# Optimization experiments

Measured on AMD Instinct MI355X. Metric: run time of the kernel, lower is better.

The kernel has to match this reference:

```python
import jax, jax.numpy as jnp
import numpy as np


def _approx_match(xyz1, xyz2):
    """Faithful port of approxmatch_cpu/cuda (auction-style soft bipartite matching).

    xyz1: [b, n, 3], xyz2: [b, m, 3] -> (match [b, n, m], sq_dists [b, n, m])
    """
    b, n, _ = xyz1.shape
    m = xyz2.shape[1]
    factorl = max(n, m) // n  # integer division, as in the CUDA source
    factorr = max(n, m) // m

    # all-pairs squared distances  [b, n, m]
    d2 = jnp.sum((xyz1[:, :, None, :] - xyz2[:, None, :, :]) ** 2, axis=-1)

    # annealing schedule: j = 8 .. -1 -> level = -4^j ; j = -2 -> level = 0
    levels = jnp.asarray([-(4.0 ** j) for j in range(8, -2, -1)] + [0.0],
                         dtype=xyz1.dtype)

    satl0 = jnp.full((b, n), float(factorl), dtype=xyz1.dtype)  # row capacities
    satr0 = jnp.full((b, m), float(factorr), dtype=xyz1.dtype)  # col capacities
    match0 = jnp.zeros((b, n, m), dtype=xyz1.dtype)

    def step(carry, level):
        satl, satr, match = carry
        # weight = exp(level * d2) * saturatedr
        w = jnp.exp(level * d2) * satr[:, None, :]                       # [b,n,m]
        # row-normalize, scale by remaining row capacity
        w = w / (jnp.sum(w, axis=2, keepdims=True) + 1e-9) * satl[:, :, None]
        # column rescale by remaining column capacity
        ss = jnp.sum(w, axis=1) + 1e-9                                   # [b,m]
        w = w * (satr / ss)[:, None, :]
        # deplete capacities
        satl = jnp.maximum(satl - jnp.sum(w, axis=2), 0.0)
        satr = jnp.maximum(satr - jnp.sum(w, axis=1), 0.0)
        return (satl, satr, match + w), None

    (_, _, match), _ = jax.lax.scan(step, (satl0, satr0, match0), levels)
    return match, d2


def setup_inputs() -> dict:
    key = jax.random.key(0)
    k1, k2 = jax.random.split(key)
    b, n, m = 4, 4096, 4096
    return {
        "input1": jax.random.normal(k1, (b, n, 3), dtype=jnp.float32),
        "input2": jax.random.normal(k2, (b, m, 3), dtype=jnp.float32),
        "eps": 0,    # accepted but unused by the original Function
        "iters": 50, # accepted but unused by the original Function
    }


def reference(input1, input2, eps, iters):
    # eps / iters are ignored, matching EarthMoverDistanceFunction.apply(xyz1, xyz2)
    match, d2 = _approx_match(input1, input2)
    dist = jnp.sqrt(jnp.maximum(d2, 1e-12))  # matchcost uses euclidean (sqrt) distance
    return jnp.sum(match * dist, axis=(1, 2))  # cost per batch element, [b]
```

## Files before the change

### kernel.cpp

```cpp
#include <hip/hip_runtime.h>

#define BLOCK 256
#define IC    64
#define RPT   4
#define ROWS  (BLOCK*RPT)
#define RBLK  64

__device__ __forceinline__ float wave_reduce_add(float v) {
#pragma unroll
    for (int off = 32; off > 0; off >>= 1) v += __shfl_down(v, off, 64);
    return v;
}
__device__ __forceinline__ float lg2(float x) { return __builtin_amdgcn_logf(x); }
__device__ __forceinline__ float ex2(float x) { return __builtin_amdgcn_exp2f(x); }

__device__ __forceinline__ void load_rows(const float* p, float* x, float* y, float* z) {
    float4 v0 = *(const float4*)p;
    float4 v1 = *(const float4*)(p + 4);
    float4 v2 = *(const float4*)(p + 8);
    x[0]=v0.x; x[1]=v0.w; x[2]=v1.z; x[3]=v2.y;
    y[0]=v0.y; y[1]=v1.x; y[2]=v1.w; y[3]=v2.z;
    z[0]=v0.z; z[1]=v1.y; z[2]=v2.x; z[3]=v2.w;
}

__global__ __launch_bounds__(BLOCK)
void emd_init(float* __restrict__ satl, float* __restrict__ satr,
              float* __restrict__ out, float fl, float fr,
              int b, int n, int m) {
    int idx = blockIdx.x * blockDim.x + threadIdx.x;
    if (idx < b * n) satl[idx] = fl;
    if (idx < b * m) satr[idx] = fr;
    if (idx < b)     out[idx]  = 0.f;
}

__global__ __launch_bounds__(BLOCK, 4)
void emd_pass1(const float* __restrict__ xyz1, const float* __restrict__ xyz2,
               float* __restrict__ P1p, float ls, float wconst, float thr,
               int n, int m, int bn)
{
    __shared__ float4 sh[IC];
    const int bb = blockIdx.z, chunk = blockIdx.y;

    const int i0 = blockIdx.x * ROWS + threadIdx.x * RPT;
    float x[RPT], y[RPT], z[RPT], acc[RPT];
    load_rows(xyz1 + ((size_t)bb * n + i0) * 3, x, y, z);

    const float* x2 = xyz2 + (size_t)bb * m * 3;
    for (int t = threadIdx.x; t < IC; t += BLOCK) {
        int j = chunk * IC + t;
        sh[t] = make_float4(x2[3*j], x2[3*j+1], x2[3*j+2], wconst);
    }
    __syncthreads();

#pragma unroll
    for (int r = 0; r < RPT; ++r) acc[r] = 0.f;
#pragma unroll 2
    for (int tb = 0; tb < IC; tb += 4) {
        float4 q0 = sh[tb+0], q1 = sh[tb+1], q2 = sh[tb+2], q3 = sh[tb+3];
        float d0[RPT], d1[RPT], d2v[RPT], d3[RPT];
        float dmin = 1e30f;
#pragma unroll
        for (int r = 0; r < RPT; ++r) {
            float dx, dy, dz;
            dx=x[r]-q0.x; dy=y[r]-q0.y; dz=z[r]-q0.z; d0[r]=fmaf(dz,dz,fmaf(dy,dy,dx*dx));
            dx=x[r]-q1.x; dy=y[r]-q1.y; dz=z[r]-q1.z; d1[r]=fmaf(dz,dz,fmaf(dy,dy,dx*dx));
            dx=x[r]-q2.x; dy=y[r]-q2.y; dz=z[r]-q2.z; d2v[r]=fmaf(dz,dz,fmaf(dy,dy,dx*dx));
            dx=x[r]-q3.x; dy=y[r]-q3.y; dz=z[r]-q3.z; d3[r]=fmaf(dz,dz,fmaf(dy,dy,dx*dx));
            dmin = fminf(dmin, fminf(fminf(d0[r], d1[r]), fminf(d2v[r], d3[r])));
        }
        if (__any(dmin < thr)) {
#pragma unroll
            for (int r = 0; r < RPT; ++r) {
                acc[r] += ex2(fmaf(d0[r],  ls, q0.w));
                acc[r] += ex2(fmaf(d1[r],  ls, q1.w));
                acc[r] += ex2(fmaf(d2v[r], ls, q2.w));
                acc[r] += ex2(fmaf(d3[r],  ls, q3.w));
            }
        }
    }
    *(float4*)&P1p[(size_t)chunk * bn + (size_t)bb * n + i0] =
        make_float4(acc[0], acc[1], acc[2], acc[3]);
}

__global__ __launch_bounds__(BLOCK, 4)
void emd_pass2(const float* __restrict__ xyzO, const float* __restrict__ xyzS,
               const float* __restrict__ satlIn, float* __restrict__ satlOut,
               const float* __restrict__ aIn, float* __restrict__ aOut,
               const float* __restrict__ P1p, const float* __restrict__ P3a,
               const float* __restrict__ P3b, float* __restrict__ P2p,
               float* __restrict__ cost,
               float ls, float thr, int nO, int nS, int bnS, int bnO,
               int C4, int first)
{
    __shared__ float4 sh[IC];
    __shared__ float red[3][4][IC];
    const int bb = blockIdx.z, chunk = blockIdx.y;

    const int j0 = blockIdx.x * ROWS + threadIdx.x * RPT;
    float x[RPT], y[RPT], z[RPT], acc[RPT];
    load_rows(xyzO + ((size_t)bb * nO + j0) * 3, x, y, z);

    const int t6 = threadIdx.x & 63, g = threadIdx.x >> 6;
    const size_t ri = (size_t)bb * nS + chunk * IC + t6;
    {
        float ps = 0.f, pa = 0.f, pb = 0.f;
        const int c0 = g * C4;
        if (first) {
#pragma unroll 16
            for (int k = 0; k < C4; ++k) ps += P1p[(size_t)(c0 + k) * bnS + ri];
        } else {
#pragma unroll 16
            for (int k = 0; k < C4; ++k) {
                ps += P1p[(size_t)(c0 + k) * bnS + ri];
                pa += P3a[(size_t)(c0 + k) * bnS + ri];
                pb += P3b[(size_t)(c0 + k) * bnS + ri];
            }
        }
        red[0][g][t6] = ps; red[1][g][t6] = pa; red[2][g][t6] = pb;
    }
    __syncthreads();
    if (threadIdx.x < IC) {
        float rs = red[0][0][t6] + red[0][1][t6] + red[0][2][t6] + red[0][3][t6];
        float sl, costv = 0.f;
        if (first) {
            sl = satlIn[ri];
        } else {
            float s1 = red[1][0][t6] + red[1][1][t6] + red[1][2][t6] + red[1][3][t6];
            float s2 = red[2][0][t6] + red[2][1][t6] + red[2][2][t6] + red[2][3][t6];
            float ap = aIn[ri];
            sl = fmaxf(satlIn[ri] - ap * s1, 0.f);
            costv = ap * s2;
        }
        float av = sl / (rs + 1e-9f);
        if (blockIdx.x == 0) {
            satlOut[ri] = sl;
            aOut[ri]    = av;
            if (!first) {
                float cv = wave_reduce_add(costv);
                if (t6 == 0) atomicAdd(&cost[bb], cv);
            }
        }
        const float* xs = xyzS + ((size_t)bb * nS + chunk * IC + t6) * 3;
        sh[t6] = make_float4(xs[0], xs[1], xs[2], lg2(av));
    }
    __syncthreads();

#pragma unroll
    for (int r = 0; r < RPT; ++r) acc[r] = 0.f;
    if (thr < 1e29f) {
#pragma unroll 2
        for (int tb = 0; tb < IC; tb += 4) {
            float4 q0 = sh[tb+0], q1 = sh[tb+1], q2 = sh[tb+2], q3 = sh[tb+3];
            float d0[RPT], d1[RPT], d2v[RPT], d3[RPT];
            float dmin = 1e30f;
#pragma unroll
            for (int r = 0; r < RPT; ++r) {
                float dx, dy, dz;
                dx=x[r]-q0.x; dy=y[r]-q0.y; dz=z[r]-q0.z; d0[r]=fmaf(dz,dz,fmaf(dy,dy,dx*dx));
                dx=x[r]-q1.x; dy=y[r]-q1.y; dz=z[r]-q1.z; d1[r]=fmaf(dz,dz,fmaf(dy,dy,dx*dx));
                dx=x[r]-q2.x; dy=y[r]-q2.y; dz=z[r]-q2.z; d2v[r]=fmaf(dz,dz,fmaf(dy,dy,dx*dx));
                dx=x[r]-q3.x; dy=y[r]-q3.y; dz=z[r]-q3.z; d3[r]=fmaf(dz,dz,fmaf(dy,dy,dx*dx));
                dmin = fminf(dmin, fminf(fminf(d0[r], d1[r]), fminf(d2v[r], d3[r])));
            }
            if (__any(dmin < thr)) {
#pragma unroll
                for (int r = 0; r < RPT; ++r) {
                    acc[r] += ex2(fmaf(d0[r],  ls, q0.w));
                    acc[r] += ex2(fmaf(d1[r],  ls, q1.w));
                    acc[r] += ex2(fmaf(d2v[r], ls, q2.w));
                    acc[r] += ex2(fmaf(d3[r],  ls, q3.w));
                }
            }
        }
    } else {
#pragma unroll 2
        for (int tb = 0; tb < IC; tb += 4) {
            float4 q0 = sh[tb+0], q1 = sh[tb+1], q2 = sh[tb+2], q3 = sh[tb+3];
#pragma unroll
            for (int r = 0; r < RPT; ++r) {
                float dx, dy, dz, d2;
                dx=x[r]-q0.x; dy=y[r]-q0.y; dz=z[r]-q0.z;
                d2=fmaf(dz,dz,fmaf(dy,dy,dx*dx)); acc[r] += ex2(fmaf(d2, ls, q0.w));
                dx=x[r]-q1.x; dy=y[r]-q1.y; dz=z[r]-q1.z;
                d2=fmaf(dz,dz,fmaf(dy,dy,dx*dx)); acc[r] += ex2(fmaf(d2, ls, q1.w));
                dx=x[r]-q2.x; dy=y[r]-q2.y; dz=z[r]-q2.z;
                d2=fmaf(dz,dz,fmaf(dy,dy,dx*dx)); acc[r] += ex2(fmaf(d2, ls, q2.w));
                dx=x[r]-q3.x; dy=y[r]-q3.y; dz=z[r]-q3.z;
                d2=fmaf(dz,dz,fmaf(dy,dy,dx*dx)); acc[r] += ex2(fmaf(d2, ls, q3.w));
            }
        }
    }
    *(float4*)&P2p[(size_t)chunk * bnO + (size_t)bb * nO + j0] =
        make_float4(acc[0], acc[1], acc[2], acc[3]);
}

__global__ __launch_bounds__(BLOCK, 4)
void emd_fused(const float* __restrict__ xyz1, const float* __restrict__ xyz2,
               const float* __restrict__ satrIn, float* __restrict__ satrOut,
               const float* __restrict__ P2p,
               float* __restrict__ P3a, float* __restrict__ P3b,
               float* __restrict__ P1p,
               float lsA, float lsB, float thr,
               int n, int m, int bn, int bm, int C4, int sumOnly)
{
    __shared__ float4 sh[IC];
    __shared__ float  shB[IC];
    __shared__ float  red[4][IC];
    __shared__ float  snsumS;
    const int bb = blockIdx.z, chunk = blockIdx.y;

    const int i0 = blockIdx.x * ROWS + threadIdx.x * RPT;
    float x[RPT], y[RPT], z[RPT];
    load_rows(xyz1 + ((size_t)bb * n + i0) * 3, x, y, z);

    const int t6 = threadIdx.x & 63, g = threadIdx.x >> 6;
    const size_t rj = (size_t)bb * m + chunk * IC + t6;
    {
        float ps = 0.f;
        const int c0 = g * C4;
#pragma unroll 16
        for (int k = 0; k < C4; ++k) ps += P2p[(size_t)(c0 + k) * bm + rj];
        red[g][t6] = ps;
    }
    __syncthreads();
    if (threadIdx.x < IC) {
        float cs  = red[0][t6] + red[1][t6] + red[2][t6] + red[3][t6];
        float sr  = satrIn[rj];
        float cs2 = sr * cs;
        float inv = sr / (cs2 + 1e-9f);
        float r2  = sr * inv;
        float sn  = fmaxf(sr - cs2 * inv, 0.f);
        if (blockIdx.x == 0) satrOut[rj] = sn;
        const float* xs = xyz2 + ((size_t)bb * m + chunk * IC + t6) * 3;
        sh[t6]  = make_float4(xs[0], xs[1], xs[2], lg2(r2));
        shB[t6] = lg2(sn);
        if (sumOnly) {
            float ss = wave_reduce_add(sn);
            if (t6 == 0) snsumS = ss;
        }
    }
    __syncthreads();

    float s1[RPT], s2[RPT], r1[RPT];
#pragma unroll
    for (int r = 0; r < RPT; ++r) { s1[r] = 0.f; s2[r] = 0.f; r1[r] = 0.f; }

    if (thr < 1e29f) {
#pragma unroll 2
        for (int tb = 0; tb < IC; tb += 4) {
            float4 q0 = sh[tb+0], q1 = sh[tb+1], q2 = sh[tb+2], q3 = sh[tb+3];
            float lb0 = shB[tb+0], lb1 = shB[tb+1], lb2 = shB[tb+2], lb3 = shB[tb+3];
            float d0[RPT], d1[RPT], d2v[RPT], d3[RPT];
            float dmin = 1e30f;
#pragma unroll
            for (int r = 0; r < RPT; ++r) {
                float dx, dy, dz;
                dx=x[r]-q0.x; dy=y[r]-q0.y; dz=z[r]-q0.z; d0[r]=fmaf(dz,dz,fmaf(dy,dy,dx*dx));
                dx=x[r]-q1.x; dy=y[r]-q1.y; dz=z[r]-q1.z; d1[r]=fmaf(dz,dz,fmaf(dy,dy,dx*dx));
                dx=x[r]-q2.x; dy=y[r]-q2.y; dz=z[r]-q2.z; d2v[r]=fmaf(dz,dz,fmaf(dy,dy,dx*dx));
                dx=x[r]-q3.x; dy=y[r]-q3.y; dz=z[r]-q3.z; d3[r]=fmaf(dz,dz,fmaf(dy,dy,dx*dx));
                dmin = fminf(dmin, fminf(fminf(d0[r], d1[r]), fminf(d2v[r], d3[r])));
            }
            if (__any(dmin < thr)) {
#pragma unroll
                for (int r = 0; r < RPT; ++r) {
                    float e;
                    e = ex2(fmaf(d0[r], lsA, q0.w));
                    s1[r] += e; s2[r] = fmaf(e, __builtin_amdgcn_sqrtf(d0[r]), s2[r]);
                    r1[r] += ex2(fmaf(d0[r], lsB, lb0));
                    e = ex2(fmaf(d1[r], lsA, q1.w));
                    s1[r] += e; s2[r] = fmaf(e, __builtin_amdgcn_sqrtf(d1[r]), s2[r]);
                    r1[r] += ex2(fmaf(d1[r], lsB, lb1));
                    e = ex2(fmaf(d2v[r], lsA, q2.w));
                    s1[r] += e; s2[r] = fmaf(e, __builtin_amdgcn_sqrtf(d2v[r]), s2[r]);
                    r1[r] += ex2(fmaf(d2v[r], lsB, lb2));
                    e = ex2(fmaf(d3[r], lsA, q3.w));
                    s1[r] += e; s2[r] = fmaf(e, __builtin_amdgcn_sqrtf(d3[r]), s2[r]);
                    r1[r] += ex2(fmaf(d3[r], lsB, lb3));
                }
            }
        }
    } else if (sumOnly) {
#pragma unroll 2
        for (int tb = 0; tb < IC; tb += 4) {
            float4 q0 = sh[tb+0], q1 = sh[tb+1], q2 = sh[tb+2], q3 = sh[tb+3];
#pragma unroll
            for (int r = 0; r < RPT; ++r) {
                float dx, dy, dz, d2, e;
                dx=x[r]-q0.x; dy=y[r]-q0.y; dz=z[r]-q0.z;
                d2=fmaf(dz,dz,fmaf(dy,dy,dx*dx));
                e = ex2(fmaf(d2, lsA, q0.w));
                s1[r] += e; s2[r] = fmaf(e, __builtin_amdgcn_sqrtf(d2), s2[r]);
                dx=x[r]-q1.x; dy=y[r]-q1.y; dz=z[r]-q1.z;
                d2=fmaf(dz,dz,fmaf(dy,dy,dx*dx));
                e = ex2(fmaf(d2, lsA, q1.w));
                s1[r] += e; s2[r] = fmaf(e, __builtin_amdgcn_sqrtf(d2), s2[r]);
                dx=x[r]-q2.x; dy=y[r]-q2.y; dz=z[r]-q2.z;
                d2=fmaf(dz,dz,fmaf(dy,dy,dx*dx));
                e = ex2(fmaf(d2, lsA, q2.w));
                s1[r] += e; s2[r] = fmaf(e, __builtin_amdgcn_sqrtf(d2), s2[r]);
                dx=x[r]-q3.x; dy=y[r]-q3.y; dz=z[r]-q3.z;
                d2=fmaf(dz,dz,fmaf(dy,dy,dx*dx));
                e = ex2(fmaf(d2, lsA, q3.w));
                s1[r] += e; s2[r] = fmaf(e, __builtin_amdgcn_sqrtf(d2), s2[r]);
            }
        }
    } else {
#pragma unroll 2
        for (int tb = 0; tb < IC; tb += 4) {
            float4 q0 = sh[tb+0], q1 = sh[tb+1], q2 = sh[tb+2], q3 = sh[tb+3];
            float lb0 = shB[tb+0], lb1 = shB[tb+1], lb2 = shB[tb+2], lb3 = shB[tb+3];
#pragma unroll
            for (int r = 0; r < RPT; ++r) {
                float dx, dy, dz, d2, e;
                dx=x[r]-q0.x; dy=y[r]-q0.y; dz=z[r]-q0.z;
                d2=fmaf(dz,dz,fmaf(dy,dy,dx*dx));
                e = ex2(fmaf(d2, lsA, q0.w));
                s1[r] += e; s2[r] = fmaf(e, __builtin_amdgcn_sqrtf(d2), s2[r]);
                r1[r] += ex2(fmaf(d2, lsB, lb0));
                dx=x[r]-q1.x; dy=y[r]-q1.y; dz=z[r]-q1.z;
                d2=fmaf(dz,dz,fmaf(dy,dy,dx*dx));
                e = ex2(fmaf(d2, lsA, q1.w));
                s1[r] += e; s2[r] = fmaf(e, __builtin_amdgcn_sqrtf(d2), s2[r]);
                r1[r] += ex2(fmaf(d2, lsB, lb1));
                dx=x[r]-q2.x; dy=y[r]-q2.y; dz=z[r]-q2.z;
                d2=fmaf(dz,dz,fmaf(dy,dy,dx*dx));
                e = ex2(fmaf(d2, lsA, q2.w));
                s1[r] += e; s2[r] = fmaf(e, __builtin_amdgcn_sqrtf(d2), s2[r]);
                r1[r] += ex2(fmaf(d2, lsB, lb2));
                dx=x[r]-q3.x; dy=y[r]-q3.y; dz=z[r]-q3.z;
                d2=fmaf(dz,dz,fmaf(dy,dy,dx*dx));
                e = ex2(fmaf(d2, lsA, q3.w));
                s1[r] += e; s2[r] = fmaf(e, __builtin_amdgcn_sqrtf(d2), s2[r]);
                r1[r] += ex2(fmaf(d2, lsB, lb3));
            }
        }
    }
    size_t base = (size_t)chunk * bn + (size_t)bb * n + i0;
    if (sumOnly) {
        float sc = snsumS;
#pragma unroll
        for (int r = 0; r < RPT; ++r) r1[r] = sc;
    }
    *(float4*)&P3a[base] = make_float4(s1[0], s1[1], s1[2], s1[3]);
    *(float4*)&P3b[base] = make_float4(s2[0], s2[1], s2[2], s2[3]);
    *(float4*)&P1p[base] = make_float4(r1[0], r1[1], r1[2], r1[3]);
}

__global__ __launch_bounds__(BLOCK, 4)
void emd_pass3_last(const float* __restrict__ xyz1, const float* __restrict__ xyz2,
                    const float* __restrict__ satrIn, const float* __restrict__ P2p,
                    float* __restrict__ P3b, int n, int m, int bn, int bm, int C4)
{
    __shared__ float4 sh[IC];
    __shared__ float red[4][IC];
    const int bb = blockIdx.z, chunk = blockIdx.y;

    const int i0 = blockIdx.x * ROWS + threadIdx.x * RPT;
    float x[RPT], y[RPT], z[RPT], s2[RPT];
    load_rows(xyz1 + ((size_t)bb * n + i0) * 3, x, y, z);

    const int t6 = threadIdx.x & 63, g = threadIdx.x >> 6;
    const size_t rj = (size_t)bb * m + chunk * IC + t6;
    {
        float ps = 0.f;
        const int c0 = g * C4;
#pragma unroll 16
        for (int k = 0; k < C4; ++k) ps += P2p[(size_t)(c0 + k) * bm + rj];
        red[g][t6] = ps;
    }
    __syncthreads();
    if (threadIdx.x < IC) {
        float cs  = red[0][t6] + red[1][t6] + red[2][t6] + red[3][t6];
        float sr  = satrIn[rj];
        float cs2 = sr * cs;
        float inv = sr / (cs2 + 1e-9f);
        const float* xs = xyz2 + ((size_t)bb * m + chunk * IC + t6) * 3;
        sh[t6] = make_float4(xs[0], xs[1], xs[2], sr * inv);
    }
    __syncthreads();

#pragma unroll
    for (int r = 0; r < RPT; ++r) s2[r] = 0.f;
#pragma unroll 4
    for (int tb = 0; tb < IC; tb += 4) {
        float4 q0 = sh[tb+0], q1 = sh[tb+1], q2 = sh[tb+2], q3 = sh[tb+3];
#pragma unroll
        for (int r = 0; r < RPT; ++r) {
            float dx, dy, dz, d2;
            dx = x[r]-q0.x; dy = y[r]-q0.y; dz = z[r]-q0.z;
            d2 = fmaf(dz, dz, fmaf(dy, dy, dx*dx));
            s2[r] = fmaf(q0.w, __builtin_amdgcn_sqrtf(d2), s2[r]);
            dx = x[r]-q1.x; dy = y[r]-q1.y; dz = z[r]-q1.z;
            d2 = fmaf(dz, dz, fmaf(dy, dy, dx*dx));
            s2[r] = fmaf(q1.w, __builtin_amdgcn_sqrtf(d2), s2[r]);
            dx = x[r]-q2.x; dy = y[r]-q2.y; dz = z[r]-q2.z;
            d2 = fmaf(dz, dz, fmaf(dy, dy, dx*dx));
            s2[r] = fmaf(q2.w, __builtin_amdgcn_sqrtf(d2), s2[r]);
            dx = x[r]-q3.x; dy = y[r]-q3.y; dz = z[r]-q3.z;
            d2 = fmaf(dz, dz, fmaf(dy, dy, dx*dx));
            s2[r] = fmaf(q3.w, __builtin_amdgcn_sqrtf(d2), s2[r]);
        }
    }
    *(float4*)&P3b[(size_t)chunk * bn + (size_t)bb * n + i0] =
        make_float4(s2[0], s2[1], s2[2], s2[3]);
}

__global__ __launch_bounds__(RBLK)
void emd_final(const float* __restrict__ a, const float* __restrict__ P3b,
               float* __restrict__ cost, int C, int bn, int n)
{
    const int idx = blockIdx.x * RBLK + threadIdx.x;
    float s2 = 0.f;
#pragma unroll 16
    for (int c = 0; c < C; ++c) s2 += P3b[(size_t)c * bn + idx];
    float cv = wave_reduce_add(a[idx] * s2);
    if (threadIdx.x == 0) atomicAdd(&cost[idx / n], cv);
}

extern "C" void kernel_launch(void* const* d_in, const int* in_sizes, int n_in,
                              void* d_out, int out_size, void* d_ws, size_t ws_size,
                              hipStream_t stream)
{
    const float* xyz1 = (const float*)d_in[0];
    const float* xyz2 = (const float*)d_in[1];
    const int b = out_size;
    const int n = in_sizes[0] / (3 * b);
    const int m = in_sizes[1] / (3 * b);
    const int C  = m / IC;
    const int C2 = n / IC;
    const int bn = b * n, bm = b * m;

    float* ws    = (float*)d_ws;
    float* satlA = ws; ws += (size_t)bn;
    float* satlB = ws; ws += (size_t)bn;
    float* satrA = ws; ws += (size_t)bm;
    float* satrB = ws; ws += (size_t)bm;
    float* aA    = ws; ws += (size_t)bn;
    float* aB    = ws; ws += (size_t)bn;
    float* P1p   = ws; ws += (size_t)bn * C;
    float* P2p   = ws; ws += (size_t)bm * C2;
    float* P3a   = ws; ws += (size_t)bn * C;
    float* P3b   = ws; ws += (size_t)bn * C;

    float* out = (float*)d_out;

    const int mx = n > m ? n : m;
    const float fl = (float)(mx / n), fr = (float)(mx / m);
    const float lgfr = log2f(fr);

    emd_init<<<dim3((b * mx + BLOCK - 1) / BLOCK), BLOCK, 0, stream>>>(
        satlA, satrA, out, fl, fr, b, n, m);

    const double LOG2E = 1.4426950408889634074;
    const double levels[11] = {-65536.0, -16384.0, -4096.0, -1024.0, -256.0,
                               -64.0, -16.0, -4.0, -1.0, -0.25, 0.0};
    float lsv[11], thrP[11], thrF[10];
    for (int k = 0; k < 11; ++k) {
        lsv[k] = (float)(levels[k] * LOG2E);
        thrP[k] = (k <= 3) ? 165.f / fabsf(lsv[k]) : 1e30f;
    }
    for (int k = 0; k < 10; ++k)
        thrF[k] = (k <= 3) ? 165.f / fabsf(lsv[k]) : 1e30f;

    const dim3 g1(n / ROWS, m / IC, b);
    const dim3 g2(m / ROWS, n / IC, b);
    const dim3 gRn(bn / RBLK);

    emd_pass1<<<g1, BLOCK, 0, stream>>>(xyz1, xyz2, P1p, lsv[0], lgfr, thrP[0],
                                        n, m, bn);

    float *slI = satlA, *slO = satlB, *aI = aA, *aO = aB;
    float *srI = satrA, *srO = satrB;
    for (int L = 0; L <= 10; ++L) {
        emd_pass2<<<g2, BLOCK, 0, stream>>>(xyz2, xyz1, slI, slO, aI, aO,
                                            P1p, P3a, P3b, P2p, out,
                                            lsv[L], thrP[L], m, n, bn, bm,
                                            C / 4, (L == 0) ? 1 : 0);
        { float* t = slI; slI = slO; slO = t; }
        { float* t = aI;  aI  = aO;  aO  = t; }
        if (L < 10) {
            emd_fused<<<g1, BLOCK, 0, stream>>>(xyz1, xyz2, srI, srO, P2p,
                                                P3a, P3b, P1p,
                                                lsv[L], lsv[L + 1], thrF[L],
                                                n, m, bn, bm, C2 / 4,
                                                (levels[L + 1] == 0.0) ? 1 : 0);
            { float* t = srI; srI = srO; srO = t; }
        } else {
            emd_pass3_last<<<g1, BLOCK, 0, stream>>>(xyz1, xyz2, srI, P2p, P3b,
                                                     n, m, bn, bm, C2 / 4);
        }
    }
    emd_final<<<gRn, RBLK, 0, stream>>>(aI, P3b, out, C, bn, n);
}
```

Baseline: 698.1 us.

## Derive next-level exponentials by squaring and replace last pairwise pass with reduction

For levels 4-8 (adjacent levels differ by a factor of 4), the fused kernel computes one exp2 at the next level and gets the current level's weight by squaring it twice. This removes one transcendental per pair. At the final level 0 the weights do not depend on distance, so the last all-pairs pass2 is replaced by a per-row reduction kernel that accumulates a per-batch sum via atomics. pass3_last then uses that sum instead of reducing the P2p partials. The squaring can underflow or lose precision compared with computing each exp directly, and the atomics add a small nondeterminism.

```diff
diff --git a/kernel.cpp b/kernel.cpp
--- a/kernel.cpp
+++ b/kernel.cpp
@@ -25,12 +25,12 @@
 
 __global__ __launch_bounds__(BLOCK)
 void emd_init(float* __restrict__ satl, float* __restrict__ satr,
-              float* __restrict__ out, float fl, float fr,
-              int b, int n, int m) {
+              float* __restrict__ out, float* __restrict__ Asum,
+              float fl, float fr, int b, int n, int m) {
     int idx = blockIdx.x * blockDim.x + threadIdx.x;
     if (idx < b * n) satl[idx] = fl;
     if (idx < b * m) satr[idx] = fr;
-    if (idx < b)     out[idx]  = 0.f;
+    if (idx < b)   { out[idx] = 0.f; Asum[idx] = 0.f; }
 }
 
 __global__ __launch_bounds__(BLOCK, 4)
@@ -201,7 +201,7 @@
                float* __restrict__ P3a, float* __restrict__ P3b,
                float* __restrict__ P1p,
                float lsA, float lsB, float thr,
-               int n, int m, int bn, int bm, int C4, int sumOnly)
+               int n, int m, int bn, int bm, int C4, int mode)
 {
     __shared__ float4 sh[IC];
     __shared__ float  shB[IC];
@@ -232,11 +232,16 @@
         float sn  = fmaxf(sr - cs2 * inv, 0.f);
         if (blockIdx.x == 0) satrOut[rj] = sn;
         const float* xs = xyz2 + ((size_t)bb * m + chunk * IC + t6) * 3;
-        sh[t6]  = make_float4(xs[0], xs[1], xs[2], lg2(r2));
-        shB[t6] = lg2(sn);
-        if (sumOnly) {
-            float ss = wave_reduce_add(sn);
-            if (t6 == 0) snsumS = ss;
+        if (mode == 0) {
+            sh[t6]  = make_float4(xs[0], xs[1], xs[2], lg2(r2));
+            shB[t6] = lg2(sn);
+        } else {
+            sh[t6]  = make_float4(xs[0], xs[1], xs[2], r2);
+            shB[t6] = sn;
+            if (mode == 2) {
+                float ss = wave_reduce_add(sn);
+                if (t6 == 0) snsumS = ss;
+            }
         }
     }
     __syncthreads();
@@ -245,7 +250,7 @@
 #pragma unroll
     for (int r = 0; r < RPT; ++r) { s1[r] = 0.f; s2[r] = 0.f; r1[r] = 0.f; }
 
-    if (thr < 1e29f) {
+    if (mode == 0) {
 #pragma unroll 2
         for (int tb = 0; tb < IC; tb += 4) {
             float4 q0 = sh[tb+0], q1 = sh[tb+1], q2 = sh[tb+2], q3 = sh[tb+3];
@@ -280,64 +285,64 @@
                 }
             }
         }
-    } else if (sumOnly) {
+    } else if (mode == 1) {
 #pragma unroll 2
         for (int tb = 0; tb < IC; tb += 4) {
             float4 q0 = sh[tb+0], q1 = sh[tb+1], q2 = sh[tb+2], q3 = sh[tb+3];
+            float lb0 = shB[tb+0], lb1 = shB[tb+1], lb2 = shB[tb+2], lb3 = shB[tb+3];
 #pragma unroll
             for (int r = 0; r < RPT; ++r) {
-                float dx, dy, dz, d2, e;
+                float dx, dy, dz, d2, t, t2, e3;
                 dx=x[r]-q0.x; dy=y[r]-q0.y; dz=z[r]-q0.z;
                 d2=fmaf(dz,dz,fmaf(dy,dy,dx*dx));
-                e = ex2(fmaf(d2, lsA, q0.w));
-                s1[r] += e; s2[r] = fmaf(e, __builtin_amdgcn_sqrtf(d2), s2[r]);
+                t = ex2(d2 * lsB); t2 = t*t; e3 = t2*t2*q0.w;
+                s1[r] += e3; s2[r] = fmaf(e3, __builtin_amdgcn_sqrtf(d2), s2[r]);
+                r1[r] = fmaf(t, lb0, r1[r]);
                 dx=x[r]-q1.x; dy=y[r]-q1.y; dz=z[r]-q1.z;
                 d2=fmaf(dz,dz,fmaf(dy,dy,dx*dx));
-                e = ex2(fmaf(d2, lsA, q1.w));
-                s1[r] += e; s2[r] = fmaf(e, __builtin_amdgcn_sqrtf(d2), s2[r]);
+                t = ex2(d2 * lsB); t2 = t*t; e3 = t2*t2*q1.w;
+                s1[r] += e3; s2[r] = fmaf(e3, __builtin_amdgcn_sqrtf(d2), s2[r]);
+                r1[r] = fmaf(t, lb1, r1[r]);
                 dx=x[r]-q2.x; dy=y[r]-q2.y; dz=z[r]-q2.z;
                 d2=fmaf(dz,dz,fmaf(dy,dy,dx*dx));
-                e = ex2(fmaf(d2, lsA, q2.w));
-                s1[r] += e; s2[r] = fmaf(e, __builtin_amdgcn_sqrtf(d2), s2[r]);
+                t = ex2(d2 * lsB); t2 = t*t; e3 = t2*t2*q2.w;
+                s1[r] += e3; s2[r] = fmaf(e3, __builtin_amdgcn_sqrtf(d2), s2[r]);
+                r1[r] = fmaf(t, lb2, r1[r]);
                 dx=x[r]-q3.x; dy=y[r]-q3.y; dz=z[r]-q3.z;
                 d2=fmaf(dz,dz,fmaf(dy,dy,dx*dx));
-                e = ex2(fmaf(d2, lsA, q3.w));
-                s1[r] += e; s2[r] = fmaf(e, __builtin_amdgcn_sqrtf(d2), s2[r]);
+                t = ex2(d2 * lsB); t2 = t*t; e3 = t2*t2*q3.w;
+                s1[r] += e3; s2[r] = fmaf(e3, __builtin_amdgcn_sqrtf(d2), s2[r]);
+                r1[r] = fmaf(t, lb3, r1[r]);
             }
         }
     } else {
 #pragma unroll 2
         for (int tb = 0; tb < IC; tb += 4) {
             float4 q0 = sh[tb+0], q1 = sh[tb+1], q2 = sh[tb+2], q3 = sh[tb+3];
-            float lb0 = shB[tb+0], lb1 = shB[tb+1], lb2 = shB[tb+2], lb3 = shB[tb+3];
 #pragma unroll
             for (int r = 0; r < RPT; ++r) {
                 float dx, dy, dz, d2, e;
                 dx=x[r]-q0.x; dy=y[r]-q0.y; dz=z[r]-q0.z;
                 d2=fmaf(dz,dz,fmaf(dy,dy,dx*dx));
-                e = ex2(fmaf(d2, lsA, q0.w));
+                e = ex2(d2 * lsA) * q0.w;
                 s1[r] += e; s2[r] = fmaf(e, __builtin_amdgcn_sqrtf(d2), s2[r]);
-                r1[r] += ex2(fmaf(d2, lsB, lb0));
                 dx=x[r]-q1.x; dy=y[r]-q1.y; dz=z[r]-q1.z;
                 d2=fmaf(dz,dz,fmaf(dy,dy,dx*dx));
-                e = ex2(fmaf(d2, lsA, q1.w));
+                e = ex2(d2 * lsA) * q1.w;
                 s1[r] += e; s2[r] = fmaf(e, __builtin_amdgcn_sqrtf(d2), s2[r]);
-                r1[r] += ex2(fmaf(d2, lsB, lb1));
                 dx=x[r]-q2.x; dy=y[r]-q2.y; dz=z[r]-q2.z;
                 d2=fmaf(dz,dz,fmaf(dy,dy,dx*dx));
-                e = ex2(fmaf(d2, lsA, q2.w));
+                e = ex2(d2 * lsA) * q2.w;
                 s1[r] += e; s2[r] = fmaf(e, __builtin_amdgcn_sqrtf(d2), s2[r]);
-                r1[r] += ex2(fmaf(d2, lsB, lb2));
                 dx=x[r]-q3.x; dy=y[r]-q3.y; dz=z[r]-q3.z;
                 d2=fmaf(dz,dz,fmaf(dy,dy,dx*dx));
-                e = ex2(fmaf(d2, lsA, q3.w));
+                e = ex2(d2 * lsA) * q3.w;
                 s1[r] += e; s2[r] = fmaf(e, __builtin_amdgcn_sqrtf(d2), s2[r]);
-                r1[r] += ex2(fmaf(d2, lsB, lb3));
             }
         }
     }
     size_t base = (size_t)chunk * bn + (size_t)bb * n + i0;
-    if (sumOnly) {
+    if (mode == 2) {
         float sc = snsumS;
 #pragma unroll
         for (int r = 0; r < RPT; ++r) r1[r] = sc;
@@ -347,36 +352,54 @@
     *(float4*)&P1p[base] = make_float4(r1[0], r1[1], r1[2], r1[3]);
 }
 
+__global__ __launch_bounds__(BLOCK)
+void emd_redL_last(const float* __restrict__ satl, const float* __restrict__ aIn,
+                   float* __restrict__ aOut,
+                   const float* __restrict__ P1p, const float* __restrict__ P3a,
+                   const float* __restrict__ P3b, float* __restrict__ cost,
+                   float* __restrict__ Asum, int C, int bn, int n)
+{
+    const int idx = blockIdx.x * BLOCK + threadIdx.x;
+    float rs = 0.f, s1 = 0.f, s2 = 0.f;
+#pragma unroll 16
+    for (int c = 0; c < C; ++c) {
+        rs += P1p[(size_t)c * bn + idx];
+        s1 += P3a[(size_t)c * bn + idx];
+        s2 += P3b[(size_t)c * bn + idx];
+    }
+    float ap = aIn[idx];
+    float sl = fmaxf(satl[idx] - ap * s1, 0.f);
+    float av = sl / (rs + 1e-9f);
+    aOut[idx] = av;
+    float cv  = wave_reduce_add(ap * s2);
+    float avs = wave_reduce_add(av);
+    if ((threadIdx.x & 63) == 0) {
+        atomicAdd(&cost[idx / n], cv);
+        atomicAdd(&Asum[idx / n], avs);
+    }
+}
+
 __global__ __launch_bounds__(BLOCK, 4)
 void emd_pass3_last(const float* __restrict__ xyz1, const float* __restrict__ xyz2,
-                    const float* __restrict__ satrIn, const float* __restrict__ P2p,
-                    float* __restrict__ P3b, int n, int m, int bn, int bm, int C4)
+                    const float* __restrict__ satrIn, const float* __restrict__ Asum,
+                    float* __restrict__ P3b, int n, int m, int bn, int bm)
 {
     __shared__ float4 sh[IC];
-    __shared__ float red[4][IC];
     const int bb = blockIdx.z, chunk = blockIdx.y;
 
     const int i0 = blockIdx.x * ROWS + threadIdx.x * RPT;
     float x[RPT], y[RPT], z[RPT], s2[RPT];
     load_rows(xyz1 + ((size_t)bb * n + i0) * 3, x, y, z);
 
-    const int t6 = threadIdx.x & 63, g = threadIdx.x >> 6;
-    const size_t rj = (size_t)bb * m + chunk * IC + t6;
-    {
-        float ps = 0.f;
-        const int c0 = g * C4;
-#pragma unroll 16
-        for (int k = 0; k < C4; ++k) ps += P2p[(size_t)(c0 + k) * bm + rj];
-        red[g][t6] = ps;
-    }
-    __syncthreads();
-    if (threadIdx.x < IC) {
-        float cs  = red[0][t6] + red[1][t6] + red[2][t6] + red[3][t6];
+    const float A = Asum[bb];
+    for (int t = threadIdx.x; t < IC; t += BLOCK) {
+        int j = chunk * IC + t;
+        size_t rj = (size_t)bb * m + j;
         float sr  = satrIn[rj];
-        float cs2 = sr * cs;
+        float cs2 = sr * A;
         float inv = sr / (cs2 + 1e-9f);
-        const float* xs = xyz2 + ((size_t)bb * m + chunk * IC + t6) * 3;
-        sh[t6] = make_float4(xs[0], xs[1], xs[2], sr * inv);
+        const float* xs = xyz2 + ((size_t)bb * m + j) * 3;
+        sh[t] = make_float4(xs[0], xs[1], xs[2], sr * inv);
     }
     __syncthreads();
 
@@ -438,6 +461,7 @@
     float* satrB = ws; ws += (size_t)bm;
     float* aA    = ws; ws += (size_t)bn;
     float* aB    = ws; ws += (size_t)bn;
+    float* Asum  = ws; ws += 16;
     float* P1p   = ws; ws += (size_t)bn * C;
     float* P2p   = ws; ws += (size_t)bm * C2;
     float* P3a   = ws; ws += (size_t)bn * C;
@@ -450,7 +474,7 @@
     const float lgfr = log2f(fr);
 
     emd_init<<<dim3((b * mx + BLOCK - 1) / BLOCK), BLOCK, 0, stream>>>(
-        satlA, satrA, out, fl, fr, b, n, m);
+        satlA, satrA, out, Asum, fl, fr, b, n, m);
 
     const double LOG2E = 1.4426950408889634074;
     const double levels[11] = {-65536.0, -16384.0, -4096.0, -1024.0, -256.0,
@@ -465,31 +489,29 @@
 
     const dim3 g1(n / ROWS, m / IC, b);
     const dim3 g2(m / ROWS, n / IC, b);
-    const dim3 gRn(bn / RBLK);
 
     emd_pass1<<<g1, BLOCK, 0, stream>>>(xyz1, xyz2, P1p, lsv[0], lgfr, thrP[0],
                                         n, m, bn);
 
     float *slI = satlA, *slO = satlB, *aI = aA, *aO = aB;
     float *srI = satrA, *srO = satrB;
-    for (int L = 0; L <= 10; ++L) {
+    for (int L = 0; L <= 9; ++L) {
         emd_pass2<<<g2, BLOCK, 0, stream>>>(xyz2, xyz1, slI, slO, aI, aO,
                                             P1p, P3a, P3b, P2p, out,
                                             lsv[L], thrP[L], m, n, bn, bm,
                                             C / 4, (L == 0) ? 1 : 0);
         { float* t = slI; slI = slO; slO = t; }
         { float* t = aI;  aI  = aO;  aO  = t; }
-        if (L < 10) {
-            emd_fused<<<g1, BLOCK, 0, stream>>>(xyz1, xyz2, srI, srO, P2p,
-                                                P3a, P3b, P1p,
-                                                lsv[L], lsv[L + 1], thrF[L],
-                                                n, m, bn, bm, C2 / 4,
-                                                (levels[L + 1] == 0.0) ? 1 : 0);
-            { float* t = srI; srI = srO; srO = t; }
-        } else {
-            emd_pass3_last<<<g1, BLOCK, 0, stream>>>(xyz1, xyz2, srI, P2p, P3b,
-                                                     n, m, bn, bm, C2 / 4);
-        }
-    }
-    emd_final<<<gRn, RBLK, 0, stream>>>(aI, P3b, out, C, bn, n);
-}
+        const int mode = (L <= 3) ? 0 : ((L <= 8) ? 1 : 2);
+        emd_fused<<<g1, BLOCK, 0, stream>>>(xyz1, xyz2, srI, srO, P2p,
+                                            P3a, P3b, P1p,
+                                            lsv[L], lsv[L + 1], thrF[L],
+                                            n, m, bn, bm, C2 / 4, mode);
+        { float* t = srI; srI = srO; srO = t; }
+    }
+    emd_redL_last<<<dim3(bn / BLOCK), BLOCK, 0, stream>>>(
+        slI, aI, aO, P1p, P3a, P3b, out, Asum, C, bn, n);
+    emd_pass3_last<<<g1, BLOCK, 0, stream>>>(xyz1, xyz2, srI, Asum, P3b,
+                                             n, m, bn, bm);
+    emd_final<<<dim3(bn / RBLK), RBLK, 0, stream>>>(aO, P3b, out, C, bn, n);
+}
```

Result: no change. 686.2 us (-1.7%).
